# Performance work log

Measured on AMD Instinct MI355X. Metric: run time of the kernel, lower is better.

Reference implementation:

```python
import jax, jax.numpy as jnp
import numpy as np

K = 7
PAD = K // 2
BN_EPS = 1e-5


def _unfold(x):
    # x: (B, C, H, W) -> (B, C, K*K, H, W), torch.F.unfold row-major kernel order
    B, C, H, W = x.shape
    xp = jnp.pad(x, ((0, 0), (0, 0), (PAD, PAD), (PAD, PAD)))
    patches = [xp[:, :, i:i + H, j:j + W] for i in range(K) for j in range(K)]
    return jnp.stack(patches, axis=2)


def setup_inputs() -> dict:
    key = jax.random.key(0)
    ks = jax.random.split(key, 6)
    B, C, H, W = 1, 256, 80, 80
    Cp = 19
    return {
        "x": jax.random.normal(ks[0], (B, C, H, W), jnp.float32),
        "coarse_probs": jax.random.uniform(ks[1], (B, Cp, H, W), jnp.float32),
        "sigma": jnp.ones((1,), jnp.float32),
        "w_feat": jax.random.normal(ks[2], (C, C), jnp.float32) * 0.05,
        "w_fuse": jax.random.normal(ks[3], (C, C), jnp.float32) * 0.05,
        "bn_gamma": jnp.ones((C,), jnp.float32),
        "bn_beta": jnp.zeros((C,), jnp.float32),
        "bn_mean": jax.random.normal(ks[4], (C,), jnp.float32) * 0.1,
        "bn_var": jax.random.uniform(ks[5], (C,), jnp.float32) + 0.5,
    }


def reference(x, coarse_probs, sigma, w_feat, w_fuse, bn_gamma, bn_beta, bn_mean, bn_var):
    # BatchNorm2d (inference, running stats)
    inv = jax.lax.rsqrt(bn_var + BN_EPS)
    xn = (x - bn_mean[None, :, None, None]) * (inv * bn_gamma)[None, :, None, None] \
         + bn_beta[None, :, None, None]

    # affinity from coarse probs over K*K neighborhood
    up = _unfold(coarse_probs)                      # (B, Cp, K2, H, W)
    center = up[:, :, (K * K - 1) // 2][:, :, None]  # (B, Cp, 1, H, W)
    dist_sq = jnp.sum((up - center) ** 2, axis=1)    # (B, K2, H, W)
    denom = 2.0 * jax.nn.relu(sigma[0]) ** 2 + 1e-8
    affinity = jax.nn.softmax(jnp.exp(-dist_sq / denom), axis=1)

    # feature_conv (1x1, no bias), unfold, weighted aggregation
    messages = jnp.einsum('oc,bchw->bohw', w_feat, xn)
    um = _unfold(messages)                           # (B, C, K2, H, W)
    agg = jnp.sum(um * affinity[:, None], axis=2)    # (B, C, H, W)

    refined = jnp.einsum('oc,bchw->bohw', w_fuse, agg)
    return x + refined
```

## Files before the change

### kernel.cpp

```cpp
#include <hip/hip_runtime.h>
#include <math.h>

#define HW_ 6400
#define C_ 256
#define CP_ 19

typedef __bf16 bf16x8 __attribute__((ext_vector_type(8)));
typedef float  f32x4  __attribute__((ext_vector_type(4)));

static __device__ __forceinline__ unsigned short f2bf(float f) {
    union { float f; unsigned int u; } x; x.f = f;
    unsigned int r = x.u + 0x7FFF + ((x.u >> 16) & 1);
    return (unsigned short)(r >> 16);
}
static __device__ __forceinline__ float bf2f(unsigned short u) {
    union { unsigned int ui; float fv; } cv;
    cv.ui = ((unsigned int)u) << 16;
    return cv.fv;
}

__global__ __launch_bounds__(256) void wgemm_kernel(
    const float* __restrict__ wfeat, const float* __restrict__ wfuse,
    const float* __restrict__ g, const float* __restrict__ be,
    const float* __restrict__ mu, const float* __restrict__ var,
    unsigned short* __restrict__ WTb, float* __restrict__ wsum)
{
    const int o = blockIdx.x, c = threadIdx.x;
    __shared__ float row[C_];
    __shared__ float red[C_];
    row[c] = wfuse[o * C_ + c];
    __syncthreads();
    float acc = 0.0f;
#pragma unroll 8
    for (int m = 0; m < C_; ++m) acc += row[m] * wfeat[m * C_ + c];
    float scale = g[c] * rsqrtf(var[c] + 1e-5f);
    float shift = be[c] - mu[c] * scale;
    WTb[o * C_ + c] = f2bf(acc * scale);
    red[c] = acc * shift;
    __syncthreads();
    for (int s = 128; s > 0; s >>= 1) {
        if (c < s) red[c] += red[c + s];
        __syncthreads();
    }
    if (c == 0) wsum[o] = red[0];
}

__global__ __launch_bounds__(256) void affinity_kernel(
    const float* __restrict__ cp, const float* __restrict__ sigma,
    unsigned short* __restrict__ affb, float* __restrict__ S)
{
    const int lane = threadIdx.x & 63;
    const int p = blockIdx.x * 4 + (threadIdx.x >> 6);
    const int h = p / 80, w = p - h * 80;
    const int k = (lane < 49) ? lane : 48;
    const int i = k / 7, j = k - i * 7;
    const int hh = h + i - 3, ww = w + j - 3;
    const bool ok = (hh >= 0) & (hh < 80) & (ww >= 0) & (ww < 80);
    const float msk = ok ? 1.0f : 0.0f;
    int q = hh * 80 + ww;
    q = min(max(q, 0), HW_ - 1);

    float s = fmaxf(sigma[0], 0.0f);
    float inv_denom = 1.0f / (2.0f * s * s + 1e-8f);

    float d = 0.0f;
#pragma unroll
    for (int c = 0; c < CP_; ++c) {
        float u = cp[c * HW_ + q];
        float ctr = __shfl(u, 24, 64);
        float t = u * msk - ctr;
        d += t * t;
    }
    float raw = __expf(-d * inv_denom);
    float e = (lane < 49) ? __expf(raw) : 0.0f;
    float einb = (ok && lane < 49) ? e : 0.0f;
    float sum = e, sumi = einb;
#pragma unroll
    for (int off = 32; off; off >>= 1) {
        sum  += __shfl_xor(sum,  off, 64);
        sumi += __shfl_xor(sumi, off, 64);
    }
    if (lane < 49) affb[k * HW_ + p] = f2bf(e / sum);
    if (lane == 0) S[p] = sumi / sum;
}

__global__ __launch_bounds__(256) void agg8_kernel(
    const float* __restrict__ x, const unsigned short* __restrict__ affb,
    unsigned short* __restrict__ aggT)
{
    const int b = blockIdx.x;
    const int pgt = b % 25, cht = b / 25;
    const int ch_l = threadIdx.x >> 5, pg_l = threadIdx.x & 31;
    const int pg = pgt * 32 + pg_l;
    const int p0 = pg * 8;
    const int h = pg / 10, w0 = (pg - (pg / 10) * 10) * 8;
    const int c = cht * 8 + ch_l;
    const float* xc = x + c * HW_;

    float acc[8] = {0.f, 0.f, 0.f, 0.f, 0.f, 0.f, 0.f, 0.f};

#pragma unroll
    for (int i = 0; i < 7; ++i) {
        int hh = h + i - 3;
        if (hh < 0 || hh >= 80) continue;
        float f[16];
        const int rb = hh * 80;
#pragma unroll
        for (int t = 0; t < 4; ++t) {
            int lin = rb + w0 - 4 + 4 * t;
            lin = min(max(lin, rb), rb + 76);
            *(float4*)&f[4 * t] = *(const float4*)&xc[lin];
        }
#pragma unroll
        for (int e = 0; e < 16; ++e) {
            int col = w0 - 4 + e;
            f[e] = (col >= 0 && col < 80) ? f[e] : 0.0f;
        }
#pragma unroll
        for (int j = 0; j < 7; ++j) {
            const int k = i * 7 + j;
            unsigned short u8[8];
            *(uint4*)u8 = *(const uint4*)&affb[k * HW_ + p0];
#pragma unroll
            for (int px = 0; px < 8; ++px)
                acc[px] += bf2f(u8[px]) * f[px + j + 1];
        }
    }

    __shared__ float so[256][9];
#pragma unroll
    for (int px = 0; px < 8; ++px) so[pg_l * 8 + px][ch_l] = acc[px];
    __syncthreads();
    const int t = threadIdx.x;
    unsigned int pk[4];
#pragma unroll
    for (int d = 0; d < 4; ++d) {
        unsigned int lo = f2bf(so[t][2 * d]);
        unsigned int hi = f2bf(so[t][2 * d + 1]);
        pk[d] = lo | (hi << 16);
    }
    const int p = pgt * 256 + t;
    *(uint4*)&aggT[p * C_ + cht * 8] = make_uint4(pk[0], pk[1], pk[2], pk[3]);
}

__global__ __launch_bounds__(256) void mfma_gemm_kernel(
    const unsigned short* __restrict__ WTb, const unsigned short* __restrict__ aggT,
    const float* __restrict__ wsum, const float* __restrict__ S,
    const float* __restrict__ x, float* __restrict__ out)
{
    const int wave = threadIdx.x >> 6, lane = threadIdx.x & 63;
    const int q = lane >> 4, l15 = lane & 15;
    const int bm = blockIdx.y * 64;
    const int n0 = blockIdx.x * 256 + wave * 64;

    f32x4 acc[4][4];
#pragma unroll
    for (int mi = 0; mi < 4; ++mi)
#pragma unroll
        for (int ni = 0; ni < 4; ++ni) acc[mi][ni] = (f32x4){0.f, 0.f, 0.f, 0.f};

#pragma unroll
    for (int k0 = 0; k0 < 256; k0 += 32) {
        bf16x8 af[4], bf[4];
#pragma unroll
        for (int mi = 0; mi < 4; ++mi)
            af[mi] = *(const bf16x8*)&WTb[(bm + mi * 16 + l15) * C_ + k0 + q * 8];
#pragma unroll
        for (int ni = 0; ni < 4; ++ni)
            bf[ni] = *(const bf16x8*)&aggT[(n0 + ni * 16 + l15) * C_ + k0 + q * 8];
#pragma unroll
        for (int mi = 0; mi < 4; ++mi)
#pragma unroll
            for (int ni = 0; ni < 4; ++ni)
                acc[mi][ni] = __builtin_amdgcn_mfma_f32_16x16x32_bf16(
                    af[mi], bf[ni], acc[mi][ni], 0, 0, 0);
    }

#pragma unroll
    for (int mi = 0; mi < 4; ++mi) {
#pragma unroll
        for (int ni = 0; ni < 4; ++ni) {
            int p = n0 + ni * 16 + l15;
            float Sp = S[p];
#pragma unroll
            for (int r = 0; r < 4; ++r) {
                int m = bm + mi * 16 + q * 4 + r;
                out[m * HW_ + p] = x[m * HW_ + p] + wsum[m] * Sp + acc[mi][ni][r];
            }
        }
    }
}

extern "C" void kernel_launch(void* const* d_in, const int* in_sizes, int n_in,
                              void* d_out, int out_size, void* d_ws, size_t ws_size,
                              hipStream_t stream) {
    const float* x      = (const float*)d_in[0];
    const float* cp     = (const float*)d_in[1];
    const float* sigma  = (const float*)d_in[2];
    const float* w_feat = (const float*)d_in[3];
    const float* w_fuse = (const float*)d_in[4];
    const float* g      = (const float*)d_in[5];
    const float* be     = (const float*)d_in[6];
    const float* mu     = (const float*)d_in[7];
    const float* var    = (const float*)d_in[8];
    float* out = (float*)d_out;

    char* wsb = (char*)d_ws;
    unsigned short* WTb  = (unsigned short*)wsb;
    unsigned short* aggT = (unsigned short*)(wsb + 131072);
    float* wsum = (float*)(wsb + 131072 + 3276800);
    float* S    = wsum + 256;
    unsigned short* affb = (unsigned short*)(S + HW_);

    wgemm_kernel<<<256, 256, 0, stream>>>(w_feat, w_fuse, g, be, mu, var, WTb, wsum);
    affinity_kernel<<<1600, 256, 0, stream>>>(cp, sigma, affb, S);
    agg8_kernel<<<800, 256, 0, stream>>>(x, affb, aggT);
    mfma_gemm_kernel<<<dim3(25, 4), 256, 0, stream>>>(WTb, aggT, wsum, S, x, out);
}
```

Before: 133.0 us.

## Merge weight GEMM with affinity and wsum with aggregation, retile output GEMM

Folds the weight-product GEMM into the affinity kernel as extra blocks and replaces the per-row GEMV with a tiled shared-memory SGEMM. The wsum reduction becomes extra blocks of the aggregation kernel, computed from the bf16 WTb, which cuts one launch. Affinity is now stored as fp32 instead of bf16, doubling its traffic. The final MFMA GEMM is retiled from 100 to 200 blocks with smaller per-wave tiles to fill more CUs. Computing wsum from bf16 weights, and dividing be by scale, may slightly change accuracy.

```diff
diff --git a/kernel.cpp b/kernel.cpp
--- a/kernel.cpp
+++ b/kernel.cpp
@@ -19,128 +19,183 @@
     return cv.fv;
 }
 
-__global__ __launch_bounds__(256) void wgemm_kernel(
+__global__ __launch_bounds__(256) void prep_kernel(
+    const float* __restrict__ cp, const float* __restrict__ sigma,
     const float* __restrict__ wfeat, const float* __restrict__ wfuse,
+    const float* __restrict__ g, const float* __restrict__ var,
+    float* __restrict__ aff, float* __restrict__ S,
+    unsigned short* __restrict__ WTb)
+{
+    if (blockIdx.x < 1600) {
+        const int lane = threadIdx.x & 63;
+        const int p = blockIdx.x * 4 + (threadIdx.x >> 6);
+        const int h = p / 80, w = p - h * 80;
+        const int k = (lane < 49) ? lane : 48;
+        const int i = k / 7, j = k - i * 7;
+        const int hh = h + i - 3, ww = w + j - 3;
+        const bool ok = (hh >= 0) & (hh < 80) & (ww >= 0) & (ww < 80);
+        const float msk = ok ? 1.0f : 0.0f;
+        int q = hh * 80 + ww;
+        q = min(max(q, 0), HW_ - 1);
+
+        float s = fmaxf(sigma[0], 0.0f);
+        float inv_denom = 1.0f / (2.0f * s * s + 1e-8f);
+
+        float d = 0.0f;
+#pragma unroll
+        for (int c = 0; c < CP_; ++c) {
+            float u = cp[c * HW_ + q];
+            float ctr = __shfl(u, 24, 64);
+            float t = u * msk - ctr;
+            d += t * t;
+        }
+        float raw = __expf(-d * inv_denom);
+        float e = (lane < 49) ? __expf(raw) : 0.0f;
+        float einb = (ok && lane < 49) ? e : 0.0f;
+        float sum = e, sumi = einb;
+#pragma unroll
+        for (int off = 32; off; off >>= 1) {
+            sum  += __shfl_xor(sum,  off, 64);
+            sumi += __shfl_xor(sumi, off, 64);
+        }
+        if (lane < 49) aff[k * HW_ + p] = e / sum;
+        if (lane == 0) S[p] = sumi / sum;
+    } else {
+        __shared__ float sA[16][65];
+        __shared__ float sB[16][64];
+        const int tb = blockIdx.x - 1600;
+        const int bm = (tb >> 2) * 64, bn = (tb & 3) * 64;
+        const int t = threadIdx.x;
+        const int arow = t >> 2, akc = (t & 3) * 4;
+        const int bkr = t >> 4, bnc = (t & 15) * 4;
+        const int ty = t >> 4, tx = t & 15;
+        float acc[4][4] = {};
+        for (int k0 = 0; k0 < C_; k0 += 16) {
+            float4 a4 = *(const float4*)&wfuse[(bm + arow) * C_ + k0 + akc];
+            sA[akc + 0][arow] = a4.x;
+            sA[akc + 1][arow] = a4.y;
+            sA[akc + 2][arow] = a4.z;
+            sA[akc + 3][arow] = a4.w;
+            *(float4*)&sB[bkr][bnc] = *(const float4*)&wfeat[(k0 + bkr) * C_ + bn + bnc];
+            __syncthreads();
+#pragma unroll
+            for (int kk = 0; kk < 16; ++kk) {
+                float a[4], b[4];
+#pragma unroll
+                for (int i = 0; i < 4; ++i) a[i] = sA[kk][ty * 4 + i];
+                *(float4*)b = *(const float4*)&sB[kk][tx * 4];
+#pragma unroll
+                for (int i = 0; i < 4; ++i)
+#pragma unroll
+                    for (int j = 0; j < 4; ++j) acc[i][j] += a[i] * b[j];
+            }
+            __syncthreads();
+        }
+        const int cbase = bn + tx * 4;
+        float sc[4];
+#pragma unroll
+        for (int j = 0; j < 4; ++j)
+            sc[j] = g[cbase + j] * rsqrtf(var[cbase + j] + 1e-5f);
+#pragma unroll
+        for (int i = 0; i < 4; ++i) {
+            const int o = bm + ty * 4 + i;
+            unsigned int lo = (unsigned int)f2bf(acc[i][0] * sc[0]) |
+                              ((unsigned int)f2bf(acc[i][1] * sc[1]) << 16);
+            unsigned int hi = (unsigned int)f2bf(acc[i][2] * sc[2]) |
+                              ((unsigned int)f2bf(acc[i][3] * sc[3]) << 16);
+            *(uint2*)&WTb[o * C_ + cbase] = make_uint2(lo, hi);
+        }
+    }
+}
+
+__global__ __launch_bounds__(256) void agg_kernel(
+    const float* __restrict__ x, const float* __restrict__ aff,
+    const unsigned short* __restrict__ WTb,
     const float* __restrict__ g, const float* __restrict__ be,
     const float* __restrict__ mu, const float* __restrict__ var,
-    unsigned short* __restrict__ WTb, float* __restrict__ wsum)
+    unsigned short* __restrict__ aggT, float* __restrict__ wsum)
 {
-    const int o = blockIdx.x, c = threadIdx.x;
-    __shared__ float row[C_];
-    __shared__ float red[C_];
-    row[c] = wfuse[o * C_ + c];
-    __syncthreads();
-    float acc = 0.0f;
-#pragma unroll 8
-    for (int m = 0; m < C_; ++m) acc += row[m] * wfeat[m * C_ + c];
-    float scale = g[c] * rsqrtf(var[c] + 1e-5f);
-    float shift = be[c] - mu[c] * scale;
-    WTb[o * C_ + c] = f2bf(acc * scale);
-    red[c] = acc * shift;
-    __syncthreads();
-    for (int s = 128; s > 0; s >>= 1) {
-        if (c < s) red[c] += red[c + s];
+    if (blockIdx.x < 800) {
+        const int b = blockIdx.x;
+        const int pgt = b % 25, cht = b / 25;
+        const int ch_l = threadIdx.x >> 5, pg_l = threadIdx.x & 31;
+        const int pg = pgt * 32 + pg_l;
+        const int p0 = pg * 8;
+        const int h = pg / 10, w0 = (pg - (pg / 10) * 10) * 8;
+        const int c = cht * 8 + ch_l;
+        const float* xc = x + c * HW_;
+
+        float acc[8] = {0.f, 0.f, 0.f, 0.f, 0.f, 0.f, 0.f, 0.f};
+
+#pragma unroll
+        for (int i = 0; i < 7; ++i) {
+            int hh = h + i - 3;
+            if (hh < 0 || hh >= 80) continue;
+            float f[16];
+            const int rb = hh * 80;
+#pragma unroll
+            for (int t = 0; t < 4; ++t) {
+                int lin = rb + w0 - 4 + 4 * t;
+                lin = min(max(lin, rb), rb + 76);
+                *(float4*)&f[4 * t] = *(const float4*)&xc[lin];
+            }
+#pragma unroll
+            for (int e = 0; e < 16; ++e) {
+                int col = w0 - 4 + e;
+                f[e] = (col >= 0 && col < 80) ? f[e] : 0.0f;
+            }
+#pragma unroll
+            for (int j = 0; j < 7; ++j) {
+                const int k = i * 7 + j;
+                float av[8];
+                *(float4*)&av[0] = *(const float4*)&aff[k * HW_ + p0];
+                *(float4*)&av[4] = *(const float4*)&aff[k * HW_ + p0 + 4];
+#pragma unroll
+                for (int px = 0; px < 8; ++px)
+                    acc[px] += av[px] * f[px + j + 1];
+            }
+        }
+
+        __shared__ float so[256][9];
+#pragma unroll
+        for (int px = 0; px < 8; ++px) so[pg_l * 8 + px][ch_l] = acc[px];
         __syncthreads();
-    }
-    if (c == 0) wsum[o] = red[0];
-}
-
-__global__ __launch_bounds__(256) void affinity_kernel(
-    const float* __restrict__ cp, const float* __restrict__ sigma,
-    unsigned short* __restrict__ affb, float* __restrict__ S)
-{
-    const int lane = threadIdx.x & 63;
-    const int p = blockIdx.x * 4 + (threadIdx.x >> 6);
-    const int h = p / 80, w = p - h * 80;
-    const int k = (lane < 49) ? lane : 48;
-    const int i = k / 7, j = k - i * 7;
-    const int hh = h + i - 3, ww = w + j - 3;
-    const bool ok = (hh >= 0) & (hh < 80) & (ww >= 0) & (ww < 80);
-    const float msk = ok ? 1.0f : 0.0f;
-    int q = hh * 80 + ww;
-    q = min(max(q, 0), HW_ - 1);
-
-    float s = fmaxf(sigma[0], 0.0f);
-    float inv_denom = 1.0f / (2.0f * s * s + 1e-8f);
-
-    float d = 0.0f;
-#pragma unroll
-    for (int c = 0; c < CP_; ++c) {
-        float u = cp[c * HW_ + q];
-        float ctr = __shfl(u, 24, 64);
-        float t = u * msk - ctr;
-        d += t * t;
-    }
-    float raw = __expf(-d * inv_denom);
-    float e = (lane < 49) ? __expf(raw) : 0.0f;
-    float einb = (ok && lane < 49) ? e : 0.0f;
-    float sum = e, sumi = einb;
-#pragma unroll
-    for (int off = 32; off; off >>= 1) {
-        sum  += __shfl_xor(sum,  off, 64);
-        sumi += __shfl_xor(sumi, off, 64);
-    }
-    if (lane < 49) affb[k * HW_ + p] = f2bf(e / sum);
-    if (lane == 0) S[p] = sumi / sum;
-}
-
-__global__ __launch_bounds__(256) void agg8_kernel(
-    const float* __restrict__ x, const unsigned short* __restrict__ affb,
-    unsigned short* __restrict__ aggT)
-{
-    const int b = blockIdx.x;
-    const int pgt = b % 25, cht = b / 25;
-    const int ch_l = threadIdx.x >> 5, pg_l = threadIdx.x & 31;
-    const int pg = pgt * 32 + pg_l;
-    const int p0 = pg * 8;
-    const int h = pg / 10, w0 = (pg - (pg / 10) * 10) * 8;
-    const int c = cht * 8 + ch_l;
-    const float* xc = x + c * HW_;
-
-    float acc[8] = {0.f, 0.f, 0.f, 0.f, 0.f, 0.f, 0.f, 0.f};
-
-#pragma unroll
-    for (int i = 0; i < 7; ++i) {
-        int hh = h + i - 3;
-        if (hh < 0 || hh >= 80) continue;
-        float f[16];
-        const int rb = hh * 80;
-#pragma unroll
-        for (int t = 0; t < 4; ++t) {
-            int lin = rb + w0 - 4 + 4 * t;
-            lin = min(max(lin, rb), rb + 76);
-            *(float4*)&f[4 * t] = *(const float4*)&xc[lin];
-        }
-#pragma unroll
-        for (int e = 0; e < 16; ++e) {
-            int col = w0 - 4 + e;
-            f[e] = (col >= 0 && col < 80) ? f[e] : 0.0f;
-        }
-#pragma unroll
-        for (int j = 0; j < 7; ++j) {
-            const int k = i * 7 + j;
+        const int t = threadIdx.x;
+        unsigned int pk[4];
+#pragma unroll
+        for (int d = 0; d < 4; ++d) {
+            unsigned int lo = f2bf(so[t][2 * d]);
+            unsigned int hi = f2bf(so[t][2 * d + 1]);
+            pk[d] = lo | (hi << 16);
+        }
+        const int p = pgt * 256 + t;
+        *(uint4*)&aggT[p * C_ + cht * 8] = make_uint4(pk[0], pk[1], pk[2], pk[3]);
+    } else {
+        __shared__ float srL[C_];
+        __shared__ float red[C_];
+        const int t = threadIdx.x;
+        {
+            float scale = g[t] * rsqrtf(var[t] + 1e-5f);
+            srL[t] = be[t] / scale - mu[t];
+        }
+        __syncthreads();
+        const int o0 = (blockIdx.x - 800) * 64;
+        const int r_l = t >> 2, seg = t & 3;
+        const int row = o0 + r_l, c0 = seg * 64;
+        float partial = 0.0f;
+#pragma unroll
+        for (int cc = 0; cc < 64; cc += 8) {
             unsigned short u8[8];
-            *(uint4*)u8 = *(const uint4*)&affb[k * HW_ + p0];
-#pragma unroll
-            for (int px = 0; px < 8; ++px)
-                acc[px] += bf2f(u8[px]) * f[px + j + 1];
-        }
-    }
-
-    __shared__ float so[256][9];
-#pragma unroll
-    for (int px = 0; px < 8; ++px) so[pg_l * 8 + px][ch_l] = acc[px];
-    __syncthreads();
-    const int t = threadIdx.x;
-    unsigned int pk[4];
-#pragma unroll
-    for (int d = 0; d < 4; ++d) {
-        unsigned int lo = f2bf(so[t][2 * d]);
-        unsigned int hi = f2bf(so[t][2 * d + 1]);
-        pk[d] = lo | (hi << 16);
-    }
-    const int p = pgt * 256 + t;
-    *(uint4*)&aggT[p * C_ + cht * 8] = make_uint4(pk[0], pk[1], pk[2], pk[3]);
+            *(uint4*)u8 = *(const uint4*)&WTb[row * C_ + c0 + cc];
+#pragma unroll
+            for (int e = 0; e < 8; ++e)
+                partial += bf2f(u8[e]) * srL[c0 + cc + e];
+        }
+        red[t] = partial;
+        __syncthreads();
+        if (t < 64)
+            wsum[o0 + t] = red[t * 4] + red[t * 4 + 1] + red[t * 4 + 2] + red[t * 4 + 3];
+    }
 }
 
 __global__ __launch_bounds__(256) void mfma_gemm_kernel(
@@ -150,26 +205,26 @@
 {
     const int wave = threadIdx.x >> 6, lane = threadIdx.x & 63;
     const int q = lane >> 4, l15 = lane & 15;
-    const int bm = blockIdx.y * 64;
-    const int n0 = blockIdx.x * 256 + wave * 64;
-
-    f32x4 acc[4][4];
-#pragma unroll
-    for (int mi = 0; mi < 4; ++mi)
+    const int m0 = blockIdx.y * 128 + wave * 32;
+    const int px0 = blockIdx.x * 64;
+
+    f32x4 acc[2][4];
+#pragma unroll
+    for (int mi = 0; mi < 2; ++mi)
 #pragma unroll
         for (int ni = 0; ni < 4; ++ni) acc[mi][ni] = (f32x4){0.f, 0.f, 0.f, 0.f};
 
 #pragma unroll
-    for (int k0 = 0; k0 < 256; k0 += 32) {
-        bf16x8 af[4], bf[4];
-#pragma unroll
-        for (int mi = 0; mi < 4; ++mi)
-            af[mi] = *(const bf16x8*)&WTb[(bm + mi * 16 + l15) * C_ + k0 + q * 8];
+    for (int k0 = 0; k0 < C_; k0 += 32) {
+        bf16x8 af[2], bf[4];
+#pragma unroll
+        for (int mi = 0; mi < 2; ++mi)
+            af[mi] = *(const bf16x8*)&WTb[(m0 + mi * 16 + l15) * C_ + k0 + q * 8];
 #pragma unroll
         for (int ni = 0; ni < 4; ++ni)
-            bf[ni] = *(const bf16x8*)&aggT[(n0 + ni * 16 + l15) * C_ + k0 + q * 8];
-#pragma unroll
-        for (int mi = 0; mi < 4; ++mi)
+            bf[ni] = *(const bf16x8*)&aggT[(px0 + ni * 16 + l15) * C_ + k0 + q * 8];
+#pragma unroll
+        for (int mi = 0; mi < 2; ++mi)
 #pragma unroll
             for (int ni = 0; ni < 4; ++ni)
                 acc[mi][ni] = __builtin_amdgcn_mfma_f32_16x16x32_bf16(
@@ -177,14 +232,14 @@
     }
 
 #pragma unroll
-    for (int mi = 0; mi < 4; ++mi) {
+    for (int mi = 0; mi < 2; ++mi) {
 #pragma unroll
         for (int ni = 0; ni < 4; ++ni) {
-            int p = n0 + ni * 16 + l15;
+            int p = px0 + ni * 16 + l15;
             float Sp = S[p];
 #pragma unroll
             for (int r = 0; r < 4; ++r) {
-                int m = bm + mi * 16 + q * 4 + r;
+                int m = m0 + mi * 16 + q * 4 + r;
                 out[m * HW_ + p] = x[m * HW_ + p] + wsum[m] * Sp + acc[mi][ni][r];
             }
         }
@@ -210,10 +265,10 @@
     unsigned short* aggT = (unsigned short*)(wsb + 131072);
     float* wsum = (float*)(wsb + 131072 + 3276800);
     float* S    = wsum + 256;
-    unsigned short* affb = (unsigned short*)(S + HW_);
-
-    wgemm_kernel<<<256, 256, 0, stream>>>(w_feat, w_fuse, g, be, mu, var, WTb, wsum);
-    affinity_kernel<<<1600, 256, 0, stream>>>(cp, sigma, affb, S);
-    agg8_kernel<<<800, 256, 0, stream>>>(x, affb, aggT);
-    mfma_gemm_kernel<<<dim3(25, 4), 256, 0, stream>>>(WTb, aggT, wsum, S, x, out);
-}
+    float* aff  = S + HW_;
+
+    prep_kernel<<<1616, 256, 0, stream>>>(cp, sigma, w_feat, w_fuse, g, var,
+                                          aff, S, WTb);
+    agg_kernel<<<804, 256, 0, stream>>>(x, aff, WTb, g, be, mu, var, aggT, wsum);
+    mfma_gemm_kernel<<<dim3(100, 2), 256, 0, stream>>>(WTb, aggT, wsum, S, x, out);
+}
```

Result: slower. 135.7 us (+2.1%).

## Merge four kernels into one cooperative persistent kernel with grid syncs

Applied to the files above, without the earlier changes.

Replaces the four separate launches with a single cooperative kernel of 512 blocks that uses two grid-wide syncs between phases. The weight-product GEMM now runs on MFMA in bf16 and overlaps with the aggregation phase on a separate set of blocks. Affinity weights are stored as fp32 rather than bf16. This removes launch gaps and the serial weight GEMM, but adds grid-sync cost and doubles the affinity traffic, and the final GEMM's tiling changes to one 16x64 tile per wave.

```diff
diff --git a/kernel.cpp b/kernel.cpp
--- a/kernel.cpp
+++ b/kernel.cpp
@@ -1,9 +1,13 @@
 #include <hip/hip_runtime.h>
+#include <hip/hip_cooperative_groups.h>
 #include <math.h>
+
+namespace cg = cooperative_groups;
 
 #define HW_ 6400
 #define C_ 256
 #define CP_ 19
+#define NBLK 512
 
 typedef __bf16 bf16x8 __attribute__((ext_vector_type(8)));
 typedef float  f32x4  __attribute__((ext_vector_type(4)));
@@ -13,179 +17,202 @@
     unsigned int r = x.u + 0x7FFF + ((x.u >> 16) & 1);
     return (unsigned short)(r >> 16);
 }
-static __device__ __forceinline__ float bf2f(unsigned short u) {
-    union { unsigned int ui; float fv; } cv;
-    cv.ui = ((unsigned int)u) << 16;
-    return cv.fv;
-}
-
-__global__ __launch_bounds__(256) void wgemm_kernel(
+
+__global__ __launch_bounds__(256, 2) void mega_kernel(
+    const float* __restrict__ cp, const float* __restrict__ sigma,
     const float* __restrict__ wfeat, const float* __restrict__ wfuse,
     const float* __restrict__ g, const float* __restrict__ be,
     const float* __restrict__ mu, const float* __restrict__ var,
-    unsigned short* __restrict__ WTb, float* __restrict__ wsum)
+    const float* __restrict__ x, float* __restrict__ out,
+    float* __restrict__ aff, float* __restrict__ S,
+    float* __restrict__ v, float* __restrict__ wsum,
+    unsigned short* __restrict__ WTb, unsigned short* __restrict__ wfuse_b,
+    unsigned short* __restrict__ wfeatT_b, unsigned short* __restrict__ aggT)
 {
-    const int o = blockIdx.x, c = threadIdx.x;
-    __shared__ float row[C_];
-    __shared__ float red[C_];
-    row[c] = wfuse[o * C_ + c];
-    __syncthreads();
-    float acc = 0.0f;
-#pragma unroll 8
-    for (int m = 0; m < C_; ++m) acc += row[m] * wfeat[m * C_ + c];
-    float scale = g[c] * rsqrtf(var[c] + 1e-5f);
-    float shift = be[c] - mu[c] * scale;
-    WTb[o * C_ + c] = f2bf(acc * scale);
-    red[c] = acc * shift;
-    __syncthreads();
-    for (int s = 128; s > 0; s >>= 1) {
-        if (c < s) red[c] += red[c + s];
-        __syncthreads();
-    }
-    if (c == 0) wsum[o] = red[0];
-}
-
-__global__ __launch_bounds__(256) void affinity_kernel(
-    const float* __restrict__ cp, const float* __restrict__ sigma,
-    unsigned short* __restrict__ affb, float* __restrict__ S)
-{
-    const int lane = threadIdx.x & 63;
-    const int p = blockIdx.x * 4 + (threadIdx.x >> 6);
-    const int h = p / 80, w = p - h * 80;
-    const int k = (lane < 49) ? lane : 48;
-    const int i = k / 7, j = k - i * 7;
-    const int hh = h + i - 3, ww = w + j - 3;
-    const bool ok = (hh >= 0) & (hh < 80) & (ww >= 0) & (ww < 80);
-    const float msk = ok ? 1.0f : 0.0f;
-    int q = hh * 80 + ww;
-    q = min(max(q, 0), HW_ - 1);
-
-    float s = fmaxf(sigma[0], 0.0f);
-    float inv_denom = 1.0f / (2.0f * s * s + 1e-8f);
-
-    float d = 0.0f;
-#pragma unroll
-    for (int c = 0; c < CP_; ++c) {
-        float u = cp[c * HW_ + q];
-        float ctr = __shfl(u, 24, 64);
-        float t = u * msk - ctr;
-        d += t * t;
-    }
-    float raw = __expf(-d * inv_denom);
-    float e = (lane < 49) ? __expf(raw) : 0.0f;
-    float einb = (ok && lane < 49) ? e : 0.0f;
-    float sum = e, sumi = einb;
-#pragma unroll
-    for (int off = 32; off; off >>= 1) {
-        sum  += __shfl_xor(sum,  off, 64);
-        sumi += __shfl_xor(sumi, off, 64);
-    }
-    if (lane < 49) affb[k * HW_ + p] = f2bf(e / sum);
-    if (lane == 0) S[p] = sumi / sum;
-}
-
-__global__ __launch_bounds__(256) void agg8_kernel(
-    const float* __restrict__ x, const unsigned short* __restrict__ affb,
-    unsigned short* __restrict__ aggT)
-{
-    const int b = blockIdx.x;
-    const int pgt = b % 25, cht = b / 25;
-    const int ch_l = threadIdx.x >> 5, pg_l = threadIdx.x & 31;
-    const int pg = pgt * 32 + pg_l;
-    const int p0 = pg * 8;
-    const int h = pg / 10, w0 = (pg - (pg / 10) * 10) * 8;
-    const int c = cht * 8 + ch_l;
-    const float* xc = x + c * HW_;
-
-    float acc[8] = {0.f, 0.f, 0.f, 0.f, 0.f, 0.f, 0.f, 0.f};
-
-#pragma unroll
-    for (int i = 0; i < 7; ++i) {
-        int hh = h + i - 3;
-        if (hh < 0 || hh >= 80) continue;
-        float f[16];
-        const int rb = hh * 80;
-#pragma unroll
-        for (int t = 0; t < 4; ++t) {
-            int lin = rb + w0 - 4 + 4 * t;
-            lin = min(max(lin, rb), rb + 76);
-            *(float4*)&f[4 * t] = *(const float4*)&xc[lin];
-        }
-#pragma unroll
-        for (int e = 0; e < 16; ++e) {
-            int col = w0 - 4 + e;
-            f[e] = (col >= 0 && col < 80) ? f[e] : 0.0f;
-        }
-#pragma unroll
-        for (int j = 0; j < 7; ++j) {
-            const int k = i * 7 + j;
-            unsigned short u8[8];
-            *(uint4*)u8 = *(const uint4*)&affb[k * HW_ + p0];
-#pragma unroll
-            for (int px = 0; px < 8; ++px)
-                acc[px] += bf2f(u8[px]) * f[px + j + 1];
-        }
-    }
+    cg::grid_group grid = cg::this_grid();
+    const int tid  = threadIdx.x;
+    const int lane = tid & 63;
+    const int wv   = tid >> 6;
+    const int gw   = blockIdx.x * 4 + wv;
+    const int gtid = blockIdx.x * 256 + tid;
+    const int q    = lane >> 4, l15 = lane & 15;
 
     __shared__ float so[256][9];
-#pragma unroll
-    for (int px = 0; px < 8; ++px) so[pg_l * 8 + px][ch_l] = acc[px];
-    __syncthreads();
-    const int t = threadIdx.x;
-    unsigned int pk[4];
-#pragma unroll
-    for (int d = 0; d < 4; ++d) {
-        unsigned int lo = f2bf(so[t][2 * d]);
-        unsigned int hi = f2bf(so[t][2 * d + 1]);
-        pk[d] = lo | (hi << 16);
-    }
-    const int p = pgt * 256 + t;
-    *(uint4*)&aggT[p * C_ + cht * 8] = make_uint4(pk[0], pk[1], pk[2], pk[3]);
-}
-
-__global__ __launch_bounds__(256) void mfma_gemm_kernel(
-    const unsigned short* __restrict__ WTb, const unsigned short* __restrict__ aggT,
-    const float* __restrict__ wsum, const float* __restrict__ S,
-    const float* __restrict__ x, float* __restrict__ out)
-{
-    const int wave = threadIdx.x >> 6, lane = threadIdx.x & 63;
-    const int q = lane >> 4, l15 = lane & 15;
-    const int bm = blockIdx.y * 64;
-    const int n0 = blockIdx.x * 256 + wave * 64;
-
-    f32x4 acc[4][4];
-#pragma unroll
-    for (int mi = 0; mi < 4; ++mi)
-#pragma unroll
-        for (int ni = 0; ni < 4; ++ni) acc[mi][ni] = (f32x4){0.f, 0.f, 0.f, 0.f};
-
-#pragma unroll
-    for (int k0 = 0; k0 < 256; k0 += 32) {
-        bf16x8 af[4], bf[4];
-#pragma unroll
-        for (int mi = 0; mi < 4; ++mi)
-            af[mi] = *(const bf16x8*)&WTb[(bm + mi * 16 + l15) * C_ + k0 + q * 8];
-#pragma unroll
-        for (int ni = 0; ni < 4; ++ni)
-            bf[ni] = *(const bf16x8*)&aggT[(n0 + ni * 16 + l15) * C_ + k0 + q * 8];
-#pragma unroll
-        for (int mi = 0; mi < 4; ++mi)
-#pragma unroll
-            for (int ni = 0; ni < 4; ++ni)
-                acc[mi][ni] = __builtin_amdgcn_mfma_f32_16x16x32_bf16(
-                    af[mi], bf[ni], acc[mi][ni], 0, 0, 0);
-    }
-
-#pragma unroll
-    for (int mi = 0; mi < 4; ++mi) {
-#pragma unroll
-        for (int ni = 0; ni < 4; ++ni) {
-            int p = n0 + ni * 16 + l15;
-            float Sp = S[p];
+
+    if (gtid < 65536) {
+        wfuse_b[gtid] = f2bf(wfuse[gtid]);
+    } else {
+        int e = gtid - 65536;
+        int m = e >> 8, c = e & 255;
+        float scale = g[c] * rsqrtf(var[c] + 1e-5f);
+        wfeatT_b[c * C_ + m] = f2bf(wfeat[e] * scale);
+    }
+    if (gw < 256) {
+        const int m = gw, c0 = lane * 4;
+        float4 wf4 = *(const float4*)&wfeat[m * C_ + c0];
+        float sh[4];
+#pragma unroll
+        for (int e = 0; e < 4; ++e) {
+            int c = c0 + e;
+            float scale = g[c] * rsqrtf(var[c] + 1e-5f);
+            sh[e] = be[c] - mu[c] * scale;
+        }
+        float part = wf4.x * sh[0] + wf4.y * sh[1] + wf4.z * sh[2] + wf4.w * sh[3];
+#pragma unroll
+        for (int off = 32; off; off >>= 1) part += __shfl_xor(part, off, 64);
+        if (lane == 0) v[m] = part;
+    }
+    for (int p = gw; p < HW_; p += 2048) {
+        const int h = p / 80, w = p - h * 80;
+        const int k = (lane < 49) ? lane : 48;
+        const int i = k / 7, j = k - i * 7;
+        const int hh = h + i - 3, ww = w + j - 3;
+        const bool ok = (hh >= 0) & (hh < 80) & (ww >= 0) & (ww < 80);
+        const float msk = ok ? 1.0f : 0.0f;
+        int qq = hh * 80 + ww;
+        qq = min(max(qq, 0), HW_ - 1);
+
+        float s = fmaxf(sigma[0], 0.0f);
+        float inv_denom = 1.0f / (2.0f * s * s + 1e-8f);
+        float d = 0.0f;
+#pragma unroll
+        for (int c = 0; c < CP_; ++c) {
+            float u = cp[c * HW_ + qq];
+            float ctr = __shfl(u, 24, 64);
+            float t = u * msk - ctr;
+            d += t * t;
+        }
+        float raw = __expf(-d * inv_denom);
+        float e = (lane < 49) ? __expf(raw) : 0.0f;
+        float einb = (ok && lane < 49) ? e : 0.0f;
+        float sum = e, sumi = einb;
+#pragma unroll
+        for (int off = 32; off; off >>= 1) {
+            sum  += __shfl_xor(sum,  off, 64);
+            sumi += __shfl_xor(sumi, off, 64);
+        }
+        if (lane < 49) aff[k * HW_ + p] = e / sum;
+        if (lane == 0) S[p] = sumi / sum;
+    }
+
+    grid.sync();
+
+    if (blockIdx.x < 496) {
+        for (int item = blockIdx.x; item < 800; item += 496) {
+            const int pgt = item % 25, cht = item / 25;
+            const int ch_l = tid >> 5, pg_l = tid & 31;
+            const int pg = pgt * 32 + pg_l;
+            const int p0 = pg * 8;
+            const int h = pg / 10, w0 = (pg - (pg / 10) * 10) * 8;
+            const int c = cht * 8 + ch_l;
+            const float* xc = x + c * HW_;
+
+            float acc[8] = {0.f, 0.f, 0.f, 0.f, 0.f, 0.f, 0.f, 0.f};
+#pragma unroll
+            for (int i = 0; i < 7; ++i) {
+                int hh = h + i - 3;
+                if (hh < 0 || hh >= 80) continue;
+                float f[16];
+                const int rb = hh * 80;
+#pragma unroll
+                for (int t = 0; t < 4; ++t) {
+                    int lin = rb + w0 - 4 + 4 * t;
+                    lin = min(max(lin, rb), rb + 76);
+                    *(float4*)&f[4 * t] = *(const float4*)&xc[lin];
+                }
+#pragma unroll
+                for (int e = 0; e < 16; ++e) {
+                    int col = w0 - 4 + e;
+                    f[e] = (col >= 0 && col < 80) ? f[e] : 0.0f;
+                }
+#pragma unroll
+                for (int j = 0; j < 7; ++j) {
+                    const int k = i * 7 + j;
+                    float av[8];
+                    *(float4*)&av[0] = *(const float4*)&aff[k * HW_ + p0];
+                    *(float4*)&av[4] = *(const float4*)&aff[k * HW_ + p0 + 4];
+#pragma unroll
+                    for (int px = 0; px < 8; ++px)
+                        acc[px] += av[px] * f[px + j + 1];
+                }
+            }
+#pragma unroll
+            for (int px = 0; px < 8; ++px) so[pg_l * 8 + px][ch_l] = acc[px];
+            __syncthreads();
+            unsigned int pk[4];
+#pragma unroll
+            for (int d = 0; d < 4; ++d) {
+                unsigned int lo = f2bf(so[tid][2 * d]);
+                unsigned int hi = f2bf(so[tid][2 * d + 1]);
+                pk[d] = lo | (hi << 16);
+            }
+            const int p = pgt * 256 + tid;
+            *(uint4*)&aggT[p * C_ + cht * 8] = make_uint4(pk[0], pk[1], pk[2], pk[3]);
+            __syncthreads();
+        }
+    } else {
+        const int tb = blockIdx.x - 496;
+        const int bo = (tb >> 2) * 64, bc = (tb & 3) * 64;
+        const int o0 = bo + wv * 16;
+        f32x4 acc[4];
+#pragma unroll
+        for (int nf = 0; nf < 4; ++nf) acc[nf] = (f32x4){0.f, 0.f, 0.f, 0.f};
+#pragma unroll
+        for (int k0 = 0; k0 < C_; k0 += 32) {
+            bf16x8 af = *(const bf16x8*)&wfuse_b[(o0 + l15) * C_ + k0 + q * 8];
+            bf16x8 bf[4];
+#pragma unroll
+            for (int nf = 0; nf < 4; ++nf)
+                bf[nf] = *(const bf16x8*)&wfeatT_b[(bc + nf * 16 + l15) * C_ + k0 + q * 8];
+#pragma unroll
+            for (int nf = 0; nf < 4; ++nf)
+                acc[nf] = __builtin_amdgcn_mfma_f32_16x16x32_bf16(af, bf[nf], acc[nf], 0, 0, 0);
+        }
+#pragma unroll
+        for (int nf = 0; nf < 4; ++nf)
+#pragma unroll
+            for (int r = 0; r < 4; ++r)
+                WTb[(o0 + q * 4 + r) * C_ + bc + nf * 16 + l15] = f2bf(acc[nf][r]);
+        const int gw2 = tb * 4 + wv;
+#pragma unroll
+        for (int rr = 0; rr < 4; ++rr) {
+            const int m = gw2 * 4 + rr, c0 = lane * 4;
+            float4 wf4 = *(const float4*)&wfuse[m * C_ + c0];
+            float4 v4  = *(const float4*)&v[c0];
+            float part = wf4.x * v4.x + wf4.y * v4.y + wf4.z * v4.z + wf4.w * v4.w;
+#pragma unroll
+            for (int off = 32; off; off >>= 1) part += __shfl_xor(part, off, 64);
+            if (lane == 0) wsum[m] = part;
+        }
+    }
+
+    grid.sync();
+
+    if (gw < 1600) {
+        const int m0 = (gw & 15) * 16;
+        const int p0 = (gw >> 4) * 64;
+        f32x4 acc[4];
+#pragma unroll
+        for (int nf = 0; nf < 4; ++nf) acc[nf] = (f32x4){0.f, 0.f, 0.f, 0.f};
+#pragma unroll
+        for (int k0 = 0; k0 < C_; k0 += 32) {
+            bf16x8 af = *(const bf16x8*)&WTb[(m0 + l15) * C_ + k0 + q * 8];
+            bf16x8 bf[4];
+#pragma unroll
+            for (int nf = 0; nf < 4; ++nf)
+                bf[nf] = *(const bf16x8*)&aggT[(p0 + nf * 16 + l15) * C_ + k0 + q * 8];
+#pragma unroll
+            for (int nf = 0; nf < 4; ++nf)
+                acc[nf] = __builtin_amdgcn_mfma_f32_16x16x32_bf16(af, bf[nf], acc[nf], 0, 0, 0);
+        }
+#pragma unroll
+        for (int nf = 0; nf < 4; ++nf) {
+            const int p = p0 + nf * 16 + l15;
+            const float Sp = S[p];
 #pragma unroll
             for (int r = 0; r < 4; ++r) {
-                int m = bm + mi * 16 + q * 4 + r;
-                out[m * HW_ + p] = x[m * HW_ + p] + wsum[m] * Sp + acc[mi][ni][r];
+                const int m = m0 + q * 4 + r;
+                out[m * HW_ + p] = x[m * HW_ + p] + wsum[m] * Sp + acc[nf][r];
             }
         }
     }
@@ -197,8 +224,8 @@
     const float* x      = (const float*)d_in[0];
     const float* cp     = (const float*)d_in[1];
     const float* sigma  = (const float*)d_in[2];
-    const float* w_feat = (const float*)d_in[3];
-    const float* w_fuse = (const float*)d_in[4];
+    const float* wfeat  = (const float*)d_in[3];
+    const float* wfuse  = (const float*)d_in[4];
     const float* g      = (const float*)d_in[5];
     const float* be     = (const float*)d_in[6];
     const float* mu     = (const float*)d_in[7];
@@ -206,14 +233,22 @@
     float* out = (float*)d_out;
 
     char* wsb = (char*)d_ws;
-    unsigned short* WTb  = (unsigned short*)wsb;
-    unsigned short* aggT = (unsigned short*)(wsb + 131072);
-    float* wsum = (float*)(wsb + 131072 + 3276800);
-    float* S    = wsum + 256;
-    unsigned short* affb = (unsigned short*)(S + HW_);
-
-    wgemm_kernel<<<256, 256, 0, stream>>>(w_feat, w_fuse, g, be, mu, var, WTb, wsum);
-    affinity_kernel<<<1600, 256, 0, stream>>>(cp, sigma, affb, S);
-    agg8_kernel<<<800, 256, 0, stream>>>(x, affb, aggT);
-    mfma_gemm_kernel<<<dim3(25, 4), 256, 0, stream>>>(WTb, aggT, wsum, S, x, out);
+    float* aff  = (float*)wsb;
+    float* S    = aff + 49 * HW_;
+    float* v    = S + HW_;
+    float* wsum = v + C_;
+    unsigned short* WTb      = (unsigned short*)(wsum + C_);
+    unsigned short* wfuse_b  = WTb + 65536;
+    unsigned short* wfeatT_b = wfuse_b + 65536;
+    unsigned short* aggT     = wfeatT_b + 65536;
+
+    void* args[] = {
+        (void*)&cp, (void*)&sigma, (void*)&wfeat, (void*)&wfuse,
+        (void*)&g, (void*)&be, (void*)&mu, (void*)&var,
+        (void*)&x, (void*)&out,
+        (void*)&aff, (void*)&S, (void*)&v, (void*)&wsum,
+        (void*)&WTb, (void*)&wfuse_b, (void*)&wfeatT_b, (void*)&aggT,
+    };
+    hipLaunchCooperativeKernel((void*)mega_kernel, dim3(NBLK), dim3(256),
+                               args, 0, stream);
 }
```

Result: slower. 271.5 us (+104.2%).
